# Kernel tuning notes

Hardware: AMD Instinct MI355X
Metric: run time of the kernel (lower is better)

Reference implementation:

```python
import jax, jax.numpy as jnp
import numpy as np

B, L, H, NH = 8, 1024, 1024, 16
HD = H // NH  # head_dim = 64
SCALE = HD ** -0.5


def setup_inputs() -> dict:
    key = jax.random.key(0)
    kx, kqkv, kw, kb = jax.random.split(key, 4)
    x = jax.random.normal(kx, (B, L, H), dtype=jnp.float32)
    # nn.Linear(H, 3H, bias=False): weight [3H, H]
    w_qkv = jax.random.normal(kqkv, (3 * H, H), dtype=jnp.float32) * (H ** -0.5)
    # out_proj: nn.Linear(H, H) with bias
    w_out = jax.random.normal(kw, (H, H), dtype=jnp.float32) * (H ** -0.5)
    b_out = jax.random.normal(kb, (H,), dtype=jnp.float32) * 0.01
    return {"x": x, "w_qkv": w_qkv, "w_out": w_out, "b_out": b_out}


def reference(x, w_qkv, w_out, b_out):
    # qkv projection: [B, L, 3H]
    qkv = jnp.einsum('bld,ed->ble', x, w_qkv)
    # rearrange 'b l (qkv h d) -> qkv b h l d'
    qkv = qkv.reshape(B, L, 3, NH, HD)
    q = qkv[:, :, 0].transpose(0, 2, 1, 3)  # [B, NH, L, HD]
    k = qkv[:, :, 1].transpose(0, 2, 1, 3)
    v = qkv[:, :, 2].transpose(0, 2, 1, 3)
    att = jnp.einsum('bhxd,bhyd->bhxy', q, k) * SCALE
    att = jax.nn.softmax(att, axis=-1)
    o = jnp.einsum('bhxy,bhyd->bhxd', att, v)  # [B, NH, L, HD]
    o = o.transpose(0, 2, 1, 3).reshape(B, L, H)
    return jnp.einsum('bld,ed->ble', o, w_out) + b_out
```

## Files before the change

### kernel.cpp

```cpp
#include <hip/hip_runtime.h>


typedef short s16x8 __attribute__((ext_vector_type(8)));
typedef float f32x4 __attribute__((ext_vector_type(4)));
typedef unsigned int u32x2 __attribute__((ext_vector_type(2)));
typedef unsigned int u32x4 __attribute__((ext_vector_type(4)));

__device__ __forceinline__ unsigned short f2bf(float f) {
    union { float f; unsigned u; } c; c.f = f;
    return (unsigned short)((c.u + 0x7FFFu + ((c.u >> 16) & 1u)) >> 16);
}
__device__ __forceinline__ unsigned pack2bf(float a, float b) {
    union { float f; unsigned u; } ca, cb; ca.f = a; cb.f = b;
    return __builtin_amdgcn_perm(cb.u + 0x8000u, ca.u + 0x8000u, 0x07060302u);
}

#define GLOAD_LDS(g, l) __builtin_amdgcn_global_load_lds( \
    (const __attribute__((address_space(1))) void*)(g),   \
    (__attribute__((address_space(3))) void*)(l), 16, 0, 0)

__global__ __launch_bounds__(256) void cvt3(
    const float* __restrict__ s0, unsigned short* __restrict__ d0, int n0,
    const float* __restrict__ s1, unsigned short* __restrict__ d1, int n1,
    const float* __restrict__ s2, unsigned short* __restrict__ d2, int n2)
{
    long i = ((long)blockIdx.x * 256 + threadIdx.x) * 8;
    const float* s; unsigned short* d; long off;
    if (i < n0)                  { s = s0; d = d0; off = i; }
    else if (i < (long)n0 + n1)  { s = s1; d = d1; off = i - n0; }
    else                         { s = s2; d = d2; off = i - n0 - n1; }
    f32x4 a = *(const f32x4*)(s + off);
    f32x4 b = *(const f32x4*)(s + off + 4);
    u32x4 r;
    r[0] = pack2bf(a[0], a[1]); r[1] = pack2bf(a[2], a[3]);
    r[2] = pack2bf(b[0], b[1]); r[3] = pack2bf(b[2], b[3]);
    *(u32x4*)(d + off) = r;
}

template<int EPI>
__global__ __launch_bounds__(256) void gemm16(
    const unsigned short* __restrict__ A, const unsigned short* __restrict__ Bm,
    unsigned short* __restrict__ Cq, unsigned short* __restrict__ Cv,
    float* __restrict__ Cf, const float* __restrict__ bias,
    int N, int K)
{
    __shared__ unsigned short As[128 * 64];
    __shared__ unsigned short Bs[128 * 64];
    const int tid = threadIdx.x, lane = tid & 63, wave = tid >> 6;
    const int quad = lane >> 4, l16 = lane & 15;
    const int wm = (wave >> 1) * 64, wn = (wave & 1) * 64;
    const int m0 = blockIdx.y * 128, n0 = blockIdx.x * 128;

    const int prow = tid >> 3;
    const int qch  = (tid & 7) ^ (prow & 7);
    const unsigned short* gA[4];
    const unsigned short* gB[4];
    #pragma unroll
    for (int c = 0; c < 4; ++c) {
        gA[c] = A + (size_t)(m0 + c * 32 + prow) * K + qch * 8;
        gB[c] = Bm + (size_t)(n0 + c * 32 + prow) * K + qch * 8;
    }
    const int sw = l16 & 7;

    f32x4 acc[4][4] = {};
    for (int k0 = 0; k0 < K; k0 += 64) {
        __syncthreads();
        #pragma unroll
        for (int c = 0; c < 4; ++c) {
            GLOAD_LDS(gA[c], As + (c * 256 + tid) * 8);
            GLOAD_LDS(gB[c], Bs + (c * 256 + tid) * 8);
            gA[c] += 64; gB[c] += 64;
        }
        __syncthreads();
        #pragma unroll
        for (int s = 0; s < 2; ++s) {
            s16x8 af[4], bf[4];
            const int pc = ((s * 4 + quad) ^ sw) * 8;
            #pragma unroll
            for (int i = 0; i < 4; ++i)
                af[i] = *(const s16x8*)(As + (wm + i * 16 + l16) * 64 + pc);
            #pragma unroll
            for (int j = 0; j < 4; ++j)
                bf[j] = *(const s16x8*)(Bs + (wn + j * 16 + l16) * 64 + pc);
            #pragma unroll
            for (int i = 0; i < 4; ++i)
                #pragma unroll
                for (int j = 0; j < 4; ++j)
                    acc[i][j] = __builtin_amdgcn_mfma_f32_16x16x32_bf16(af[i], bf[j], acc[i][j], 0, 0, 0);
        }
    }

    if (EPI == 1) {
        #pragma unroll
        for (int j = 0; j < 4; ++j) {
            int col = n0 + wn + j * 16 + l16;
            float bv = bias[col];
            #pragma unroll
            for (int i = 0; i < 4; ++i)
                #pragma unroll
                for (int r = 0; r < 4; ++r)
                    Cf[(size_t)(m0 + wm + i * 16 + quad * 4 + r) * N + col] = acc[i][j][r] + bv;
        }
    } else if (n0 < 2048) {
        const float qs = (n0 < 1024) ? 0.18033688f : 1.0f;
        #pragma unroll
        for (int j = 0; j < 4; ++j) {
            int col = n0 + wn + j * 16 + l16;
            #pragma unroll
            for (int i = 0; i < 4; ++i)
                #pragma unroll
                for (int r = 0; r < 4; ++r)
                    Cq[(size_t)(m0 + wm + i * 16 + quad * 4 + r) * 2048 + col] = f2bf(acc[i][j][r] * qs);
        }
    } else {
        #pragma unroll
        for (int j = 0; j < 4; ++j) {
            int dcol = n0 + wn + j * 16 + l16 - 2048;
            int hh = dcol >> 6, dd = dcol & 63;
            #pragma unroll
            for (int i = 0; i < 4; ++i) {
                int row = m0 + wm + i * 16 + quad * 4;
                int bb = row >> 10, l = row & 1023;
                u32x2 pw;
                pw[0] = pack2bf(acc[i][j][0], acc[i][j][1]);
                pw[1] = pack2bf(acc[i][j][2], acc[i][j][3]);
                *(u32x2*)(Cv + (size_t)((bb * 16 + hh) * 64 + dd) * 1024 + l) = pw;
            }
        }
    }
}

__global__ __launch_bounds__(256) void attn(
    const unsigned short* __restrict__ qk, const unsigned short* __restrict__ Vt,
    unsigned short* __restrict__ O)
{
    __shared__ unsigned short Ks[64 * 64];
    __shared__ unsigned short Vs[64 * 64];

    const int bh = blockIdx.y, b = bh >> 4, hh = bh & 15;
    const int q0 = blockIdx.x * 64;
    const int tid = threadIdx.x, lane = tid & 63, wave = tid >> 6;
    const int quad = lane >> 4, l16 = lane & 15;

    const unsigned short* qrow =
        qk + (size_t)(b * 1024 + q0 + wave * 16 + l16) * 2048 + hh * 64;
    s16x8 qf[2];
    qf[0] = *(const s16x8*)(qrow + quad * 8);
    qf[1] = *(const s16x8*)(qrow + 32 + quad * 8);

    const int rl = lane >> 3;
    const int qc = (lane & 7) ^ rl;
    const int u0 = rl >> 2, r0 = rl & 3;
    const int kvbase = 32 * (wave >> 1) + 4 * (wave & 1) + r0;
    const int kv0 = kvbase + 8 * u0;
    const int kv1 = kvbase + 8 * (2 + u0);
    const unsigned short* srcK0 = qk + (size_t)(b * 1024 + kv0) * 2048 + 1024 + hh * 64 + qc * 8;
    const unsigned short* srcK1 = qk + (size_t)(b * 1024 + kv1) * 2048 + 1024 + hh * 64 + qc * 8;
    const unsigned short* srcV0 = Vt + (size_t)(bh * 64 + wave * 16 + rl) * 1024 + qc * 8;
    const unsigned short* srcV1 = Vt + (size_t)(bh * 64 + wave * 16 + 8 + rl) * 1024 + qc * 8;
    unsigned short* dK0 = Ks + (wave * 16 + rl) * 64 + (lane & 7) * 8;
    unsigned short* dK1 = Ks + (wave * 16 + 8 + rl) * 64 + (lane & 7) * 8;
    unsigned short* dV0 = Vs + (wave * 16 + rl) * 64 + (lane & 7) * 8;
    unsigned short* dV1 = Vs + (wave * 16 + 8 + rl) * 64 + (lane & 7) * 8;

    const int sw = l16 & 7;

    f32x4 Oacc[4] = {};
    float lsum = 0.0f;

    for (int kv = 0; kv < 1024; kv += 64) {
        __syncthreads();
        GLOAD_LDS(srcK0, dK0);
        GLOAD_LDS(srcK1, dK1);
        GLOAD_LDS(srcV0, dV0);
        GLOAD_LDS(srcV1, dV1);
        srcK0 += (size_t)64 * 2048; srcK1 += (size_t)64 * 2048;
        srcV0 += 64; srcV1 += 64;
        __syncthreads();

        f32x4 Sacc[4] = {};
        #pragma unroll
        for (int t = 0; t < 4; ++t) {
            #pragma unroll
            for (int s = 0; s < 2; ++s) {
                s16x8 kf = *(const s16x8*)(Ks + (t * 16 + l16) * 64 + ((s * 4 + quad) ^ sw) * 8);
                Sacc[t] = __builtin_amdgcn_mfma_f32_16x16x32_bf16(kf, qf[s], Sacc[t], 0, 0, 0);
            }
        }
        unsigned upw[4][2];
        #pragma unroll
        for (int t = 0; t < 4; ++t) {
            float p0 = __builtin_amdgcn_exp2f(Sacc[t][0]);
            float p1 = __builtin_amdgcn_exp2f(Sacc[t][1]);
            float p2 = __builtin_amdgcn_exp2f(Sacc[t][2]);
            float p3 = __builtin_amdgcn_exp2f(Sacc[t][3]);
            lsum += (p0 + p1) + (p2 + p3);
            upw[t][0] = pack2bf(p0, p1);
            upw[t][1] = pack2bf(p2, p3);
        }
        #pragma unroll
        for (int s = 0; s < 2; ++s) {
            u32x4 aw;
            aw[0] = upw[2 * s][0];     aw[1] = upw[2 * s][1];
            aw[2] = upw[2 * s + 1][0]; aw[3] = upw[2 * s + 1][1];
            s16x8 pf;
            __builtin_memcpy(&pf, &aw, 16);
            #pragma unroll
            for (int jd = 0; jd < 4; ++jd) {
                s16x8 vf = *(const s16x8*)(Vs + (jd * 16 + l16) * 64 + ((s * 4 + quad) ^ sw) * 8);
                Oacc[jd] = __builtin_amdgcn_mfma_f32_16x16x32_bf16(pf, vf, Oacc[jd], 0, 0, 0);
            }
        }
    }

    lsum += __shfl_xor(lsum, 16, 64);
    lsum += __shfl_xor(lsum, 32, 64);
    float rinv[4];
    #pragma unroll
    for (int r = 0; r < 4; ++r)
        rinv[r] = 1.0f / __shfl(lsum, quad * 4 + r, 64);
    #pragma unroll
    for (int j = 0; j < 4; ++j)
        #pragma unroll
        for (int r = 0; r < 4; ++r) {
            int row = q0 + wave * 16 + quad * 4 + r;
            int col = hh * 64 + j * 16 + l16;
            O[(size_t)(b * 1024 + row) * 1024 + col] = f2bf(Oacc[j][r] * rinv[r]);
        }
}

extern "C" void kernel_launch(void* const* d_in, const int* in_sizes, int n_in,
                              void* d_out, int out_size, void* d_ws, size_t ws_size,
                              hipStream_t stream) {
    const float* x     = (const float*)d_in[0];
    const float* w_qkv = (const float*)d_in[1];
    const float* w_out = (const float*)d_in[2];
    const float* b_out = (const float*)d_in[3];
    float* out = (float*)d_out;

    const int nx = 8192 * 1024, nwq = 3072 * 1024, nwo = 1024 * 1024;
    unsigned short* xb  = (unsigned short*)d_ws;
    unsigned short* wqb = xb + nx;
    unsigned short* wob = wqb + nwq;
    unsigned short* qkb = wob + nwo;
    unsigned short* Vt  = qkb + (size_t)8192 * 2048;
    unsigned short* Ob  = xb;

    dim3 blk(256);
    cvt3<<<6144, blk, 0, stream>>>(x, xb, nx, w_qkv, wqb, nwq, w_out, wob, nwo);
    gemm16<0><<<dim3(24, 64), blk, 0, stream>>>(xb, wqb, qkb, Vt, nullptr, nullptr, 3072, 1024);
    attn<<<dim3(16, 128), blk, 0, stream>>>(qkb, Vt, Ob);
    gemm16<1><<<dim3(8, 64), blk, 0, stream>>>(Ob, wob, nullptr, nullptr, out, b_out, 1024, 1024);
}
```

Before: 234.2 us.

## Switch attention to 32x32x16 MFMA with 128-query blocks per workgroup

The attention kernel now uses the 32x32x16 bf16 MFMA instead of 16x16x32, and each wave owns 32 query rows, so a workgroup covers 128 queries and the grid is halved. Each K/V tile loaded into LDS is reused across twice as many queries, which cuts global and LDS traffic per unit of work. K rows are permuted on load to match the 32x32 output layout, so P can feed the PV MFMA directly from registers. The cost is fewer workgroups (1024) and more accumulator registers per lane, which may lower occupancy.

```diff
diff --git a/kernel.cpp b/kernel.cpp
--- a/kernel.cpp
+++ b/kernel.cpp
@@ -3,6 +3,7 @@
 
 typedef short s16x8 __attribute__((ext_vector_type(8)));
 typedef float f32x4 __attribute__((ext_vector_type(4)));
+typedef float f32x16 __attribute__((ext_vector_type(16)));
 typedef unsigned int u32x2 __attribute__((ext_vector_type(2)));
 typedef unsigned int u32x4 __attribute__((ext_vector_type(4)));
 
@@ -138,34 +139,34 @@
     __shared__ unsigned short Vs[64 * 64];
 
     const int bh = blockIdx.y, b = bh >> 4, hh = bh & 15;
-    const int q0 = blockIdx.x * 64;
+    const int q0 = blockIdx.x * 128;
     const int tid = threadIdx.x, lane = tid & 63, wave = tid >> 6;
-    const int quad = lane >> 4, l16 = lane & 15;
+    const int l31 = lane & 31, hf = lane >> 5;
 
     const unsigned short* qrow =
-        qk + (size_t)(b * 1024 + q0 + wave * 16 + l16) * 2048 + hh * 64;
-    s16x8 qf[2];
-    qf[0] = *(const s16x8*)(qrow + quad * 8);
-    qf[1] = *(const s16x8*)(qrow + 32 + quad * 8);
-
-    const int rl = lane >> 3;
-    const int qc = (lane & 7) ^ rl;
-    const int u0 = rl >> 2, r0 = rl & 3;
-    const int kvbase = 32 * (wave >> 1) + 4 * (wave & 1) + r0;
-    const int kv0 = kvbase + 8 * u0;
-    const int kv1 = kvbase + 8 * (2 + u0);
-    const unsigned short* srcK0 = qk + (size_t)(b * 1024 + kv0) * 2048 + 1024 + hh * 64 + qc * 8;
-    const unsigned short* srcK1 = qk + (size_t)(b * 1024 + kv1) * 2048 + 1024 + hh * 64 + qc * 8;
-    const unsigned short* srcV0 = Vt + (size_t)(bh * 64 + wave * 16 + rl) * 1024 + qc * 8;
-    const unsigned short* srcV1 = Vt + (size_t)(bh * 64 + wave * 16 + 8 + rl) * 1024 + qc * 8;
-    unsigned short* dK0 = Ks + (wave * 16 + rl) * 64 + (lane & 7) * 8;
-    unsigned short* dK1 = Ks + (wave * 16 + 8 + rl) * 64 + (lane & 7) * 8;
-    unsigned short* dV0 = Vs + (wave * 16 + rl) * 64 + (lane & 7) * 8;
-    unsigned short* dV1 = Vs + (wave * 16 + 8 + rl) * 64 + (lane & 7) * 8;
-
-    const int sw = l16 & 7;
-
-    f32x4 Oacc[4] = {};
+        qk + (size_t)(b * 1024 + q0 + wave * 32 + l31) * 2048 + hh * 64;
+    s16x8 qf[4];
+    #pragma unroll
+    for (int c = 0; c < 4; ++c)
+        qf[c] = *(const s16x8*)(qrow + c * 16 + hf * 8);
+
+    const int r0 = tid >> 3,        p0 = tid & 7;
+    const int r1 = r0 + 32,         p1 = p0;
+    const int qc0 = p0 ^ (r0 & 7),  qc1 = p1 ^ (r1 & 7);
+    const int kvp0 = (r0 & ~12) | ((r0 & 4) << 1) | ((r0 & 8) >> 1);
+    const int kvp1 = (r1 & ~12) | ((r1 & 4) << 1) | ((r1 & 8) >> 1);
+    const unsigned short* srcK0 = qk + (size_t)(b * 1024 + kvp0) * 2048 + 1024 + hh * 64 + qc0 * 8;
+    const unsigned short* srcK1 = qk + (size_t)(b * 1024 + kvp1) * 2048 + 1024 + hh * 64 + qc1 * 8;
+    const unsigned short* srcV0 = Vt + (size_t)(bh * 64 + r0) * 1024 + qc0 * 8;
+    const unsigned short* srcV1 = Vt + (size_t)(bh * 64 + r1) * 1024 + qc1 * 8;
+    unsigned short* dK0 = Ks + r0 * 64 + p0 * 8;
+    unsigned short* dK1 = Ks + r1 * 64 + p1 * 8;
+    unsigned short* dV0 = Vs + r0 * 64 + p0 * 8;
+    unsigned short* dV1 = Vs + r1 * 64 + p1 * 8;
+
+    const int sw = l31 & 7;
+
+    f32x16 Oacc[2] = {};
     float lsum = 0.0f;
 
     for (int kv = 0; kv < 1024; kv += 64) {
@@ -178,55 +179,55 @@
         srcV0 += 64; srcV1 += 64;
         __syncthreads();
 
-        f32x4 Sacc[4] = {};
-        #pragma unroll
-        for (int t = 0; t < 4; ++t) {
-            #pragma unroll
-            for (int s = 0; s < 2; ++s) {
-                s16x8 kf = *(const s16x8*)(Ks + (t * 16 + l16) * 64 + ((s * 4 + quad) ^ sw) * 8);
-                Sacc[t] = __builtin_amdgcn_mfma_f32_16x16x32_bf16(kf, qf[s], Sacc[t], 0, 0, 0);
-            }
-        }
-        unsigned upw[4][2];
-        #pragma unroll
-        for (int t = 0; t < 4; ++t) {
-            float p0 = __builtin_amdgcn_exp2f(Sacc[t][0]);
-            float p1 = __builtin_amdgcn_exp2f(Sacc[t][1]);
-            float p2 = __builtin_amdgcn_exp2f(Sacc[t][2]);
-            float p3 = __builtin_amdgcn_exp2f(Sacc[t][3]);
-            lsum += (p0 + p1) + (p2 + p3);
-            upw[t][0] = pack2bf(p0, p1);
-            upw[t][1] = pack2bf(p2, p3);
-        }
-        #pragma unroll
-        for (int s = 0; s < 2; ++s) {
+        f32x16 Sacc[2] = {};
+        #pragma unroll
+        for (int c = 0; c < 4; ++c) {
+            #pragma unroll
+            for (int t = 0; t < 2; ++t) {
+                s16x8 kf = *(const s16x8*)(Ks + (t * 32 + l31) * 64 + ((2 * c + hf) ^ sw) * 8);
+                Sacc[t] = __builtin_amdgcn_mfma_f32_32x32x16_bf16(kf, qf[c], Sacc[t], 0, 0, 0);
+            }
+        }
+        unsigned upw[2][8];
+        #pragma unroll
+        for (int t = 0; t < 2; ++t)
+            #pragma unroll
+            for (int i = 0; i < 8; ++i) {
+                float pa = __builtin_amdgcn_exp2f(Sacc[t][2 * i]);
+                float pb = __builtin_amdgcn_exp2f(Sacc[t][2 * i + 1]);
+                lsum += pa + pb;
+                upw[t][i] = pack2bf(pa, pb);
+            }
+        #pragma unroll
+        for (int c = 0; c < 4; ++c) {
             u32x4 aw;
-            aw[0] = upw[2 * s][0];     aw[1] = upw[2 * s][1];
-            aw[2] = upw[2 * s + 1][0]; aw[3] = upw[2 * s + 1][1];
+            aw[0] = upw[c >> 1][4 * (c & 1) + 0];
+            aw[1] = upw[c >> 1][4 * (c & 1) + 1];
+            aw[2] = upw[c >> 1][4 * (c & 1) + 2];
+            aw[3] = upw[c >> 1][4 * (c & 1) + 3];
             s16x8 pf;
             __builtin_memcpy(&pf, &aw, 16);
             #pragma unroll
-            for (int jd = 0; jd < 4; ++jd) {
-                s16x8 vf = *(const s16x8*)(Vs + (jd * 16 + l16) * 64 + ((s * 4 + quad) ^ sw) * 8);
-                Oacc[jd] = __builtin_amdgcn_mfma_f32_16x16x32_bf16(pf, vf, Oacc[jd], 0, 0, 0);
-            }
-        }
-    }
-
-    lsum += __shfl_xor(lsum, 16, 64);
+            for (int dt = 0; dt < 2; ++dt) {
+                s16x8 vf = *(const s16x8*)(Vs + (dt * 32 + l31) * 64 + ((2 * c + hf) ^ sw) * 8);
+                Oacc[dt] = __builtin_amdgcn_mfma_f32_32x32x16_bf16(pf, vf, Oacc[dt], 0, 0, 0);
+            }
+        }
+    }
+
     lsum += __shfl_xor(lsum, 32, 64);
-    float rinv[4];
+
     #pragma unroll
-    for (int r = 0; r < 4; ++r)
-        rinv[r] = 1.0f / __shfl(lsum, quad * 4 + r, 64);
-    #pragma unroll
-    for (int j = 0; j < 4; ++j)
-        #pragma unroll
-        for (int r = 0; r < 4; ++r) {
-            int row = q0 + wave * 16 + quad * 4 + r;
-            int col = hh * 64 + j * 16 + l16;
-            O[(size_t)(b * 1024 + row) * 1024 + col] = f2bf(Oacc[j][r] * rinv[r]);
-        }
+    for (int r = 0; r < 16; ++r) {
+        int q_r = (r & 3) + 8 * (r >> 2) + 4 * hf;
+        float rinv = 1.0f / __shfl(lsum, q_r, 64);
+        int row = b * 1024 + q0 + wave * 32 + q_r;
+        #pragma unroll
+        for (int dt = 0; dt < 2; ++dt) {
+            int col = hh * 64 + dt * 32 + l31;
+            O[(size_t)row * 1024 + col] = f2bf(Oacc[dt][r] * rinv);
+        }
+    }
 }
 
 extern "C" void kernel_launch(void* const* d_in, const int* in_sizes, int n_in,
@@ -249,6 +250,6 @@
     dim3 blk(256);
     cvt3<<<6144, blk, 0, stream>>>(x, xb, nx, w_qkv, wqb, nwq, w_out, wob, nwo);
     gemm16<0><<<dim3(24, 64), blk, 0, stream>>>(xb, wqb, qkb, Vt, nullptr, nullptr, 3072, 1024);
-    attn<<<dim3(16, 128), blk, 0, stream>>>(qkb, Vt, Ob);
+    attn<<<dim3(8, 128), blk, 0, stream>>>(qkb, Vt, Ob);
     gemm16<1><<<dim3(8, 64), blk, 0, stream>>>(Ob, wob, nullptr, nullptr, out, b_out, 1024, 1024);
 }
```

Result: no change. 238.7 us (+1.9%).
